# Performance work log

Measured on AMD Instinct MI355X. Metric: run time of the kernel, lower is better.

The kernel has to match this reference:

```python
import jax, jax.numpy as jnp
import numpy as np

B, H, L, D = 8, 8, 2048, 64
FACTOR = 5


def _num_sel(length):
    return min(int(FACTOR * np.ceil(np.log(length))), length)


def setup_inputs() -> dict:
    key = jax.random.key(0)
    kq, kk, kv, ki = jax.random.split(key, 4)
    num_k = _num_sel(L)
    return {
        "q": jax.random.normal(kq, (B, H, L, D), dtype=jnp.float32),
        "k": jax.random.normal(kk, (B, H, L, D), dtype=jnp.float32),
        "v": jax.random.normal(kv, (B, H, L, D), dtype=jnp.float32),
        "random_index": jax.random.randint(ki, (L, num_k), 0, L, dtype=jnp.int32),
    }


def reference(q, k, v, random_index):
    b, h, q_len, d = q.shape
    k_len = k.shape[2]
    num_q = _num_sel(q_len)

    # --- random K sampling per query: k_s[b,h,i,j,:] = k[b,h,random_index[i,j],:]
    k_s = k[:, :, random_index, :]                      # (B,H,L,num_k,D)
    pre_attn = jnp.einsum('bhid,bhijd->bhij', q, k_s)   # (B,H,L,num_k)
    measure = pre_attn.max(-1) - pre_attn.sum(-1) / k_len  # (B,H,L)

    # --- top-k query selection (sorted=False in torch; order-insensitive math)
    _, idx = jax.lax.top_k(measure, num_q)              # (B,H,num_q)
    q_sel = jnp.take_along_axis(q, idx[..., None], axis=2)  # (B,H,num_q,D)

    # --- reduced attention over all keys
    attn = jnp.einsum('bhid,bhjd->bhij', q_sel, k) * (d ** -0.5)  # (B,H,num_q,k_len)

    # ProbMask: causal mask per selected query index (mask where j > idx[i])
    mask = jnp.arange(k_len)[None, None, None, :] > idx[..., None]
    attn = jnp.where(mask, -jnp.inf, attn)
    attn = jax.nn.softmax(attn, axis=-1)

    out_sel = jnp.einsum('bhij,bhjd->bhid', attn, v)    # (B,H,num_q,D)

    # --- context initialization (use_mask=True branch) and scatter back
    context = jnp.cumsum(v, axis=2)                     # (B,H,L,D)
    bi = jnp.arange(b)[:, None, None]
    hi = jnp.arange(h)[None, :, None]
    out = context.at[bi, hi, idx].set(out_sel)          # (B,H,L,D)
    return out, attn
```

## Files before the change

kernel.cpp:

```cpp
#include <hip/hip_runtime.h>
#include <float.h>
#include <math.h>

#define B_  8
#define H_  8
#define L_  2048
#define D_  64
#define NS  40
#define BH  (B_*H_)
#define SCALE 0.125f


template<int CTRL>
__device__ __forceinline__ float dpp_add(float x) {
    int s = __builtin_amdgcn_update_dpp(0, __float_as_int(x), CTRL, 0xF, 0xF, true);
    return x + __int_as_float(s);
}

__global__ __launch_bounds__(256) void measure_kernel(
    const float* __restrict__ q, const float* __restrict__ k,
    const int* __restrict__ ridx, float* __restrict__ measure)
{
    int wave = threadIdx.x >> 6, lane = threadIdx.x & 63;
    int b = blockIdx.x;
    int xcd = b & 7, s = b >> 3;
    int bh  = xcd + ((s >> 9) << 3);
    int i   = (s & 511) * 4 + wave;
    int oct = lane >> 3;
    int e   = lane & 7;

    int rr[5];
    #pragma unroll
    for (int p = 0; p < 5; ++p) rr[p] = ridx[i * NS + p * 8 + oct];

    const float4* kb = (const float4*)(k + (size_t)bh * L_ * D_);
    const float4* qp = (const float4*)(q + ((size_t)bh * L_ + i) * D_);
    float4 qa = qp[e];
    float4 qb = qp[e + 8];

    float mx = -FLT_MAX, sm = 0.f;
    #pragma unroll
    for (int p = 0; p < 5; ++p) {
        int base = rr[p] << 4;
        float4 ka = kb[base + e];
        float4 kc = kb[base + 8 + e];
        float pa = qa.x*ka.x + qa.y*ka.y + qa.z*ka.z + qa.w*ka.w;
        float pb = qb.x*kc.x + qb.y*kc.y + qb.z*kc.z + qb.w*kc.w;
        float pp = pa + pb;
        pp = dpp_add<0x111>(pp);
        pp = dpp_add<0x112>(pp);
        pp = dpp_add<0x114>(pp);
        mx = fmaxf(mx, pp);
        sm += pp;
    }
    mx = fmaxf(mx, __shfl_xor(mx,  8, 64));  sm += __shfl_xor(sm,  8, 64);
    mx = fmaxf(mx, __shfl_xor(mx, 16, 64));  sm += __shfl_xor(sm, 16, 64);
    mx = fmaxf(mx, __shfl_xor(mx, 32, 64));  sm += __shfl_xor(sm, 32, 64);
    if (lane == 7)
        measure[(size_t)bh * L_ + i] = mx - sm * (1.0f / (float)L_);
}

__global__ __launch_bounds__(256) void topk_kernel(
    const float* __restrict__ measure, int* __restrict__ idxOut)
{
    __shared__ float wv[4]; __shared__ int wi[4];
    __shared__ float bvS;   __shared__ int biS;
    int b = blockIdx.x;
    int bh = (b & 7) + ((b >> 3) << 3);
    int t = threadIdx.x;
    const float4* m4 = (const float4*)(measure + (size_t)bh * L_);
    float vals[8];
    float4 a = m4[t*2], bb = m4[t*2 + 1];
    vals[0]=a.x; vals[1]=a.y; vals[2]=a.z; vals[3]=a.w;
    vals[4]=bb.x; vals[5]=bb.y; vals[6]=bb.z; vals[7]=bb.w;

    float lv = -FLT_MAX; int li = t*8;
    #pragma unroll
    for (int e = 0; e < 8; ++e) if (vals[e] > lv) { lv = vals[e]; li = t*8 + e; }

    int lane = t & 63, w = t >> 6;
    for (int r = 0; r < NS; ++r) {
        float v = lv; int idx = li;
        #pragma unroll
        for (int off = 32; off; off >>= 1) {
            float ov = __shfl_xor(v, off, 64);
            int   oi = __shfl_xor(idx, off, 64);
            if (ov > v || (ov == v && oi < idx)) { v = ov; idx = oi; }
        }
        if (lane == 0) { wv[w] = v; wi[w] = idx; }
        __syncthreads();
        if (t == 0) {
            float bv = wv[0]; int bi = wi[0];
            #pragma unroll
            for (int ww = 1; ww < 4; ++ww)
                if (wv[ww] > bv || (wv[ww] == bv && wi[ww] < bi)) { bv = wv[ww]; bi = wi[ww]; }
            bvS = bv; biS = bi;
            idxOut[bh * NS + r] = bi;
        }
        __syncthreads();
        int bi = biS;
        if ((bi >> 3) == t) {
            #pragma unroll
            for (int e = 0; e < 8; ++e) if ((bi & 7) == e) vals[e] = -FLT_MAX;
            lv = -FLT_MAX; li = t*8;
            #pragma unroll
            for (int e = 0; e < 8; ++e) if (vals[e] > lv) { lv = vals[e]; li = t*8 + e; }
        }
        __syncthreads();
    }
}

__global__ __launch_bounds__(256) void cumsum_p1(
    const float* __restrict__ v, float4* __restrict__ vpart)
{
    __shared__ float4 part[16][16];
    int b = blockIdx.x;
    int xcd = b & 7, s = b >> 3;
    int bh = xcd + ((s >> 4) << 3);
    int c  = s & 15;
    int d4 = threadIdx.x & 15, sub = threadIdx.x >> 4;
    const float4* vb = (const float4*)(v + (size_t)bh * L_ * D_);
    int r0 = c*128 + sub*8;
    float4 acc = make_float4(0,0,0,0);
    #pragma unroll
    for (int r = 0; r < 8; ++r) {
        float4 x = vb[(r0 + r)*16 + d4];
        acc.x += x.x; acc.y += x.y; acc.z += x.z; acc.w += x.w;
    }
    part[sub][d4] = acc;
    __syncthreads();
    if (sub == 0) {
        float4 tot = part[0][d4];
        #pragma unroll
        for (int ss = 1; ss < 16; ++ss) {
            float4 x = part[ss][d4];
            tot.x += x.x; tot.y += x.y; tot.z += x.z; tot.w += x.w;
        }
        vpart[(bh*16 + c)*16 + d4] = tot;
    }
}

__global__ __launch_bounds__(256) void cumsum_p2(
    const float* __restrict__ v, const float4* __restrict__ vpart,
    float* __restrict__ out)
{
    __shared__ float4 part[16][16];
    int b = blockIdx.x;
    int xcd = b & 7, s = b >> 3;
    int bh = xcd + ((s >> 4) << 3);
    int c  = s & 15;
    int d4 = threadIdx.x & 15, sub = threadIdx.x >> 4;
    const float4* vb = (const float4*)(v + (size_t)bh * L_ * D_);
    float4*       ob = (float4*)(out + (size_t)bh * L_ * D_);
    int r0 = c*128 + sub*8;
    float4 acc = make_float4(0,0,0,0);
    #pragma unroll
    for (int r = 0; r < 8; ++r) {
        float4 x = vb[(r0 + r)*16 + d4];
        acc.x += x.x; acc.y += x.y; acc.z += x.z; acc.w += x.w;
    }
    part[sub][d4] = acc;
    float4 run = make_float4(0,0,0,0);
    for (int cc = 0; cc < c; ++cc) {
        float4 x = vpart[(bh*16 + cc)*16 + d4];
        run.x += x.x; run.y += x.y; run.z += x.z; run.w += x.w;
    }
    __syncthreads();
    #pragma unroll
    for (int ss = 0; ss < 16; ++ss) {
        if (ss < sub) {
            float4 x = part[ss][d4];
            run.x += x.x; run.y += x.y; run.z += x.z; run.w += x.w;
        }
    }
    #pragma unroll
    for (int r = 0; r < 8; ++r) {
        float4 x = vb[(r0 + r)*16 + d4];
        run.x += x.x; run.y += x.y; run.z += x.z; run.w += x.w;
        ob[(r0 + r)*16 + d4] = run;
    }
}

__global__ __launch_bounds__(256) void scores_kernel(
    const float* __restrict__ q, const float* __restrict__ k,
    const int* __restrict__ idxSel, float* __restrict__ attn)
{
    __shared__ float4 kbuf[16 * 129];
    int b = blockIdx.x;
    int xcd = b & 7, s = b >> 3;
    int bh  = xcd + ((s / 10) << 3);
    int grp = s % 10;
    int qi = threadIdx.x >> 6, sub = threadIdx.x & 63;
    int rank = grp*4 + qi;
    int qrow = idxSel[bh*NS + rank];

    const float4* qrp = (const float4*)(q + ((size_t)bh * L_ + qrow) * D_);
    float4 qreg[16];
    #pragma unroll
    for (int g = 0; g < 16; ++g) qreg[g] = qrp[g];

    const float4* kb = (const float4*)(k + (size_t)bh * L_ * D_);
    float sc0[16], sc1[16];

    #pragma unroll
    for (int c = 0; c < 16; ++c) {
        __syncthreads();
        int j0 = c * 128;
        #pragma unroll
        for (int it = 0; it < 8; ++it) {
            int fi = threadIdx.x + 256*it;
            int g = fi & 15, j = fi >> 4;
            kbuf[g*129 + j] = kb[(size_t)(j0 + j)*16 + g];
        }
        __syncthreads();
        float acc0 = 0.f, acc1 = 0.f;
        #pragma unroll
        for (int g = 0; g < 16; ++g) {
            float4 k0 = kbuf[g*129 + sub];
            float4 k1 = kbuf[g*129 + sub + 64];
            float4 qq = qreg[g];
            acc0 += qq.x*k0.x + qq.y*k0.y + qq.z*k0.z + qq.w*k0.w;
            acc1 += qq.x*k1.x + qq.y*k1.y + qq.z*k1.z + qq.w*k1.w;
        }
        sc0[c] = acc0 * SCALE;
        sc1[c] = acc1 * SCALE;
    }

    float mx = -FLT_MAX;
    #pragma unroll
    for (int c = 0; c < 16; ++c) {
        if (c*128 + sub      <= qrow) mx = fmaxf(mx, sc0[c]);
        if (c*128 + sub + 64 <= qrow) mx = fmaxf(mx, sc1[c]);
    }
    #pragma unroll
    for (int off = 32; off; off >>= 1) mx = fmaxf(mx, __shfl_xor(mx, off, 64));

    float sum = 0.f;
    #pragma unroll
    for (int c = 0; c < 16; ++c) {
        sc0[c] = (c*128 + sub      <= qrow) ? __expf(sc0[c] - mx) : 0.f;
        sc1[c] = (c*128 + sub + 64 <= qrow) ? __expf(sc1[c] - mx) : 0.f;
        sum += sc0[c] + sc1[c];
    }
    #pragma unroll
    for (int off = 32; off; off >>= 1) sum += __shfl_xor(sum, off, 64);
    float inv = 1.f / sum;

    float* arow = attn + (size_t)(bh*NS + rank) * L_;
    #pragma unroll
    for (int c = 0; c < 16; ++c) {
        arow[c*128 + sub]      = sc0[c] * inv;
        arow[c*128 + sub + 64] = sc1[c] * inv;
    }
}

__global__ __launch_bounds__(256) void pv_kernel(
    const float* __restrict__ v, const int* __restrict__ idxSel,
    const float* __restrict__ attn, float* __restrict__ out)
{
    __shared__ float wl[4][L_ + 64];
    __shared__ float4 part[16][16];
    __shared__ int qr4[4];
    int b = blockIdx.x;
    int xcd = b & 7, s = b >> 3;
    int bh  = xcd + ((s / 10) << 3);
    int grp = s % 10;
    int t = threadIdx.x;
    if (t < 4) qr4[t] = idxSel[bh*NS + grp*4 + t];

    #pragma unroll
    for (int it = 0; it < 8; ++it) {
        int f = t + 256*it;
        int rr = f >> 9, fi = f & 511;
        const float4* ar = (const float4*)(attn + (size_t)(bh*NS + grp*4 + rr) * L_);
        float4 x = ar[fi];
        int j = 4*fi;
        *((float4*)&wl[rr][j + 4*(j >> 7)]) = x;
    }
    __syncthreads();

    int maxq = max(max(qr4[0], qr4[1]), max(qr4[2], qr4[3]));
    int d4 = t & 15, seg = t >> 4;
    const float4* vb = (const float4*)(v + (size_t)bh * L_ * D_);
    float4 acc[4];
    #pragma unroll
    for (int rr = 0; rr < 4; ++rr) acc[rr] = make_float4(0,0,0,0);

    int jlo = seg*128, jhi = min(jlo + 127, maxq);
    for (int j = jlo; j <= jhi; ++j) {
        float4 x = vb[(size_t)j*16 + d4];
        int jp = j + 4*(j >> 7);
        #pragma unroll
        for (int rr = 0; rr < 4; ++rr) {
            float wgt = wl[rr][jp];
            acc[rr].x += wgt*x.x; acc[rr].y += wgt*x.y;
            acc[rr].z += wgt*x.z; acc[rr].w += wgt*x.w;
        }
    }

    #pragma unroll
    for (int rr = 0; rr < 4; ++rr) {
        part[seg][d4] = acc[rr];
        __syncthreads();
        float4 a = acc[rr];
        for (int s2 = 8; s2; s2 >>= 1) {
            if (seg < s2) {
                float4 o = part[seg + s2][d4];
                a.x += o.x; a.y += o.y; a.z += o.z; a.w += o.w;
                part[seg][d4] = a;
            }
            __syncthreads();
        }
        if (seg == 0) {
            float4* orow = (float4*)(out + ((size_t)bh * L_ + qr4[rr]) * D_);
            orow[d4] = a;
        }
        __syncthreads();
    }
}

extern "C" void kernel_launch(void* const* d_in, const int* in_sizes, int n_in,
                              void* d_out, int out_size, void* d_ws, size_t ws_size,
                              hipStream_t stream) {
    const float* q    = (const float*)d_in[0];
    const float* k    = (const float*)d_in[1];
    const float* v    = (const float*)d_in[2];
    const int*   ridx = (const int*)d_in[3];

    float* out     = (float*)d_out;
    float* attnOut = out + (size_t)BH * L_ * D_;

    float*  measure = (float*)d_ws;
    int*    idxSel  = (int*)((char*)d_ws + (size_t)BH * L_ * sizeof(float));
    float4* vpart   = (float4*)d_ws;

    measure_kernel<<<BH * L_ / 4, 256, 0, stream>>>(q, k, ridx, measure);
    topk_kernel   <<<BH,          256, 0, stream>>>(measure, idxSel);
    cumsum_p1     <<<BH * 16,     256, 0, stream>>>(v, vpart);
    cumsum_p2     <<<BH * 16,     256, 0, stream>>>(v, vpart, out);
    scores_kernel <<<BH * 10,     256, 0, stream>>>(q, k, idxSel, attnOut);
    pv_kernel     <<<BH * 10,     256, 0, stream>>>(v, idxSel, attnOut, out);
}
```

Baseline: 326.3 us.

## Fuse two-pass cumsum into single kernel and vectorize random index loads

Replaces the two-kernel cumsum (per-chunk partial sums, then a prefix pass) with one kernel. Each block owns one (b,h) slice and 16 feature columns across the full sequence, and builds the prefix over 64 row-chunks in shared memory. This removes a launch and the workspace round trip. The measure kernel now reads the random indices with one int4 load plus a scalar instead of five scalar loads, which permutes which sampled keys each lane group handles; max and sum do not depend on that order. The fused cumsum launches only 256 blocks, and each row access covers 64-byte segments, which may hurt memory-bandwidth utilisation.

```diff
diff --git a/kernel.cpp b/kernel.cpp
--- a/kernel.cpp
+++ b/kernel.cpp
@@ -29,9 +29,9 @@
     int oct = lane >> 3;
     int e   = lane & 7;
 
-    int rr[5];
-    #pragma unroll
-    for (int p = 0; p < 5; ++p) rr[p] = ridx[i * NS + p * 8 + oct];
+    int4 r4 = *(const int4*)(ridx + i * NS + oct * 4);
+    int  r5 = ridx[i * NS + 32 + oct];
+    int rr[5] = { r4.x, r4.y, r4.z, r4.w, r5 };
 
     const float4* kb = (const float4*)(k + (size_t)bh * L_ * D_);
     const float4* qp = (const float4*)(q + ((size_t)bh * L_ + i) * D_);
@@ -110,74 +110,40 @@
     }
 }
 
-__global__ __launch_bounds__(256) void cumsum_p1(
-    const float* __restrict__ v, float4* __restrict__ vpart)
-{
-    __shared__ float4 part[16][16];
+__global__ __launch_bounds__(256) void cumsum_fused(
+    const float* __restrict__ v, float* __restrict__ out)
+{
+    __shared__ float4 part[64][5];
     int b = blockIdx.x;
     int xcd = b & 7, s = b >> 3;
-    int bh = xcd + ((s >> 4) << 3);
-    int c  = s & 15;
-    int d4 = threadIdx.x & 15, sub = threadIdx.x >> 4;
-    const float4* vb = (const float4*)(v + (size_t)bh * L_ * D_);
-    int r0 = c*128 + sub*8;
-    float4 acc = make_float4(0,0,0,0);
-    #pragma unroll
-    for (int r = 0; r < 8; ++r) {
-        float4 x = vb[(r0 + r)*16 + d4];
-        acc.x += x.x; acc.y += x.y; acc.z += x.z; acc.w += x.w;
-    }
-    part[sub][d4] = acc;
-    __syncthreads();
-    if (sub == 0) {
-        float4 tot = part[0][d4];
-        #pragma unroll
-        for (int ss = 1; ss < 16; ++ss) {
-            float4 x = part[ss][d4];
-            tot.x += x.x; tot.y += x.y; tot.z += x.z; tot.w += x.w;
-        }
-        vpart[(bh*16 + c)*16 + d4] = tot;
-    }
-}
-
-__global__ __launch_bounds__(256) void cumsum_p2(
-    const float* __restrict__ v, const float4* __restrict__ vpart,
-    float* __restrict__ out)
-{
-    __shared__ float4 part[16][16];
-    int b = blockIdx.x;
-    int xcd = b & 7, s = b >> 3;
-    int bh = xcd + ((s >> 4) << 3);
-    int c  = s & 15;
-    int d4 = threadIdx.x & 15, sub = threadIdx.x >> 4;
+    int bh  = xcd + ((s >> 2) << 3);
+    int cg  = s & 3;
+    int col = threadIdx.x & 3, sub = threadIdx.x >> 2;
+    int c0 = cg*4 + col;
+    int r0 = sub * 32;
     const float4* vb = (const float4*)(v + (size_t)bh * L_ * D_);
     float4*       ob = (float4*)(out + (size_t)bh * L_ * D_);
-    int r0 = c*128 + sub*8;
+
     float4 acc = make_float4(0,0,0,0);
     #pragma unroll
-    for (int r = 0; r < 8; ++r) {
-        float4 x = vb[(r0 + r)*16 + d4];
+    for (int r = 0; r < 32; ++r) {
+        float4 x = vb[(size_t)(r0 + r)*16 + c0];
         acc.x += x.x; acc.y += x.y; acc.z += x.z; acc.w += x.w;
     }
-    part[sub][d4] = acc;
+    part[sub][col] = acc;
+    __syncthreads();
+
     float4 run = make_float4(0,0,0,0);
-    for (int cc = 0; cc < c; ++cc) {
-        float4 x = vpart[(bh*16 + cc)*16 + d4];
+    for (int cc = 0; cc < sub; ++cc) {
+        float4 x = part[cc][col];
         run.x += x.x; run.y += x.y; run.z += x.z; run.w += x.w;
     }
-    __syncthreads();
-    #pragma unroll
-    for (int ss = 0; ss < 16; ++ss) {
-        if (ss < sub) {
-            float4 x = part[ss][d4];
-            run.x += x.x; run.y += x.y; run.z += x.z; run.w += x.w;
-        }
-    }
-    #pragma unroll
-    for (int r = 0; r < 8; ++r) {
-        float4 x = vb[(r0 + r)*16 + d4];
+
+    #pragma unroll
+    for (int r = 0; r < 32; ++r) {
+        float4 x = vb[(size_t)(r0 + r)*16 + c0];
         run.x += x.x; run.y += x.y; run.z += x.z; run.w += x.w;
-        ob[(r0 + r)*16 + d4] = run;
+        ob[(size_t)(r0 + r)*16 + c0] = run;
     }
 }
 
@@ -332,12 +298,10 @@
 
     float*  measure = (float*)d_ws;
     int*    idxSel  = (int*)((char*)d_ws + (size_t)BH * L_ * sizeof(float));
-    float4* vpart   = (float4*)d_ws;
 
     measure_kernel<<<BH * L_ / 4, 256, 0, stream>>>(q, k, ridx, measure);
     topk_kernel   <<<BH,          256, 0, stream>>>(measure, idxSel);
-    cumsum_p1     <<<BH * 16,     256, 0, stream>>>(v, vpart);
-    cumsum_p2     <<<BH * 16,     256, 0, stream>>>(v, vpart, out);
+    cumsum_fused  <<<BH * 4,      256, 0, stream>>>(v, out);
     scores_kernel <<<BH * 10,     256, 0, stream>>>(q, k, idxSel, attnOut);
     pv_kernel     <<<BH * 10,     256, 0, stream>>>(v, idxSel, attnOut, out);
 }
```

Result: no change. 325.9 us (-0.1%).
